# Kernel tuning notes

Measured on AMD Instinct MI355X. Metric: run time of the kernel, lower is better.

The kernel has to match this reference:

```python
import jax, jax.numpy as jnp
import numpy as np

B, N, D, H, E = 8, 2048, 128, 256, 524288
EPS = 1e-5

def setup_inputs() -> dict:
    key = jax.random.key(0)
    ks = jax.random.split(key, 16)
    def lin(k, fan_in, shape):
        b = 1.0 / np.sqrt(fan_in)
        return jax.random.uniform(k, shape, jnp.float32, -b, b)
    return {
        'x': jax.random.normal(ks[0], (B, N, 3), jnp.float32),
        'h': jax.random.normal(ks[1], (B, N, D), jnp.float32),
        'edge_indices': jax.random.randint(ks[2], (2, E), 0, B * N, jnp.int64),
        'batch_size': B,
        # filter_net: Linear(1,H) -> SiLU -> Linear(H,D)   (weights stored [in,out])
        'W1': lin(ks[3], 1, (1, H)), 'b1': lin(ks[4], 1, (H,)),
        'W2': lin(ks[5], H, (H, D)), 'b2': lin(ks[6], H, (D,)),
        # update_net: Linear(2D,H) -> LayerNorm(H) -> SiLU -> Linear(H,D)
        'W3': lin(ks[7], 2 * D, (2 * D, H)), 'b3': lin(ks[8], 2 * D, (H,)),
        'gamma': jnp.ones((H,), jnp.float32), 'beta': jnp.zeros((H,), jnp.float32),
        'W4': lin(ks[9], H, (H, D)), 'b4': lin(ks[10], H, (D,)),
    }

def reference(x, h, edge_indices, batch_size, W1, b1, W2, b2, W3, b3, gamma, beta, W4, b4):
    Bn, Nn, Dn = h.shape
    row, col = edge_indices[0], edge_indices[1]
    br, nr = row // Nn, row % Nn
    bc, nc = col // Nn, col % Nn
    x_row = x[br, nr]            # [E,3] gather
    x_col = x[bc, nc]            # [E,3]
    h_col = h[bc, nc]            # [E,D]
    diff = x_row - x_col
    dist = jnp.sqrt(jnp.sum(diff * diff, axis=-1, keepdims=True))  # [E,1]
    # distance-conditioned edge filter MLP
    edge_filters = jax.nn.silu(dist @ W1 + b1) @ W2 + b2           # [E,D]
    messages = h_col * edge_filters                                 # [E,D]
    # scatter-mean into B*N nodes (single-pass sum + count, clamp_min(1))
    n_tot = Bn * Nn
    sums = jax.ops.segment_sum(messages, row, num_segments=n_tot)
    counts = jax.ops.segment_sum(jnp.ones_like(row, dtype=messages.dtype), row, num_segments=n_tot)
    agg = (sums / jnp.maximum(counts, 1.0)[:, None]).reshape(Bn, Nn, Dn)
    # update MLP with LayerNorm
    u = jnp.concatenate([h, agg], axis=-1) @ W3 + b3               # [B,N,H]
    mu = jnp.mean(u, axis=-1, keepdims=True)
    var = jnp.mean((u - mu) ** 2, axis=-1, keepdims=True)
    un = (u - mu) * jax.lax.rsqrt(var + EPS) * gamma + beta
    return jax.nn.silu(un) @ W4 + b4                                # [B,N,D]
```

## Files before the change

kernel.cpp:

```cpp
#include <hip/hip_runtime.h>
#include <hip/hip_fp16.h>
#include <math.h>

#define BN_NODES 16384
#define DIM 128
#define HID 256
#define TK 4096
#define TRANGE 32.0f
#define TSTEP (TRANGE / (float)TK)
#define TINV  ((float)TK / TRANGE)
#define LN_EPS 1e-5f
#define EPB 4096
#define NBINS 1024
#define CAPB 768

typedef _Float16 f16x8 __attribute__((ext_vector_type(8)));
typedef __attribute__((ext_vector_type(4))) float f32x4;
typedef __attribute__((ext_vector_type(2))) float floatx2;
typedef __attribute__((ext_vector_type(8))) unsigned short ushort8v;

__device__ __forceinline__ unsigned short f2h(float f) {
    _Float16 h = (_Float16)f;
    return *(unsigned short*)&h;
}
__device__ __forceinline__ __half2 u2h2(unsigned int u) {
    union { unsigned int u; __half2 h; } c; c.u = u; return c.h;
}

__device__ __forceinline__ void edge_acc(unsigned int rec, int dd,
        const unsigned char* __restrict__ xq,
        const unsigned short* __restrict__ Tb, float& a0, float& a1) {
    int c = (int)((rec >> 12) & 0x3FFFu);
    int k = (int)(rec & 0xFFFu);
    unsigned short hq = *(const unsigned short*)&xq[c * DIM + dd];
    unsigned int tv = *(const unsigned int*)&Tb[k * DIM + dd];
    floatx2 hf = __builtin_amdgcn_cvt_pk_f32_fp8((int)hq, false);
    __half2 th = u2h2(tv);
    a0 = fmaf(hf[0], __low2float(th), a0);
    a1 = fmaf(hf[1], __high2float(th), a1);
}

__device__ __forceinline__ void node_tail(const unsigned int* lrec, int from, int to,
        int dd, const unsigned char* __restrict__ xq,
        const unsigned short* __restrict__ Tb, float& a0, float& a1) {
    int i = from;
    for (; i + 4 <= to; i += 4) {
        unsigned int e0 = lrec[i], e1 = lrec[i + 1], e2 = lrec[i + 2], e3 = lrec[i + 3];
        edge_acc(e0, dd, xq, Tb, a0, a1);
        edge_acc(e1, dd, xq, Tb, a0, a1);
        edge_acc(e2, dd, xq, Tb, a0, a1);
        edge_acc(e3, dd, xq, Tb, a0, a1);
    }
    for (; i < to; ++i) edge_acc(lrec[i], dd, xq, Tb, a0, a1);
}

__global__ __launch_bounds__(256) void prep_kernel(
        const float* __restrict__ W1, const float* __restrict__ b1,
        const float* __restrict__ W2, const float* __restrict__ b2,
        const float* __restrict__ W3, const float* __restrict__ W4,
        const float* __restrict__ h, const int* __restrict__ ei,
        const float* __restrict__ x,
        unsigned short* __restrict__ Tb, unsigned short* __restrict__ w3t,
        unsigned short* __restrict__ w4t, unsigned short* __restrict__ xh,
        unsigned char* __restrict__ xq, int* __restrict__ bin_cursor,
        unsigned int* __restrict__ staging, int nE) {
    __shared__ float smem[8 * 256 + 8 * 128];
    int bid = blockIdx.x, t = threadIdx.x;
    if (bid < 512) {
        float* a    = smem;
        float* part = smem + 8 * 256;
        int k0 = bid * 8;
        float w1 = W1[t], bb = b1[t];
#pragma unroll
        for (int k = 0; k < 8; ++k) {
            float dist = ((float)(k0 + k) + 0.5f) * TSTEP;
            float z = dist * w1 + bb;
            a[k * 256 + t] = z / (1.0f + expf(-z));
        }
        __syncthreads();
        int hg = t >> 7, d = t & 127;
        float acc[8] = {0.f,0.f,0.f,0.f,0.f,0.f,0.f,0.f};
        for (int hh = 0; hh < 128; ++hh) {
            int hidx = hg * 128 + hh;
            float w = W2[hidx * DIM + d];
#pragma unroll
            for (int k = 0; k < 8; ++k) acc[k] += a[k * 256 + hidx] * w;
        }
        if (hg == 1) {
#pragma unroll
            for (int k = 0; k < 8; ++k) part[k * 128 + d] = acc[k];
        }
        __syncthreads();
        if (hg == 0) {
            float bd = b2[d];
#pragma unroll
            for (int k = 0; k < 8; ++k)
                Tb[(k0 + k) * DIM + d] = f2h(acc[k] + part[k * 128 + d] + bd);
        }
    } else if (bid < 576) {
        float* s = smem;
        int tid = bid - 512, tr = tid >> 3, tc = tid & 7;
        int lr = t >> 5, lc = t & 31;
#pragma unroll
        for (int rep = 0; rep < 4; ++rep) {
            int k = tr * 32 + rep * 8 + lr, n = tc * 32 + lc;
            s[lc * 33 + rep * 8 + lr] = W3[k * 256 + n];
        }
        __syncthreads();
#pragma unroll
        for (int rep = 0; rep < 4; ++rep) {
            int n = tc * 32 + rep * 8 + lr, k = tr * 32 + lc;
            w3t[n * 256 + k] = f2h(s[(rep * 8 + lr) * 33 + lc]);
        }
    } else if (bid < 608) {
        float* s = smem;
        int tid = bid - 576, tr = tid >> 2, tc = tid & 3;
        int lr = t >> 5, lc = t & 31;
#pragma unroll
        for (int rep = 0; rep < 4; ++rep) {
            int k = tr * 32 + rep * 8 + lr, n = tc * 32 + lc;
            s[lc * 33 + rep * 8 + lr] = W4[k * 128 + n];
        }
        __syncthreads();
#pragma unroll
        for (int rep = 0; rep < 4; ++rep) {
            int n = tc * 32 + rep * 8 + lr, k = tr * 32 + lc;
            w4t[n * 256 + k] = f2h(s[(rep * 8 + lr) * 33 + lc]);
        }
    } else if (bid < 1632) {
        int i0 = (bid - 608) * 2048 + t * 8;
        float4 v0 = *(const float4*)&h[i0];
        float4 v1 = *(const float4*)&h[i0 + 4];
        ushort8v o;
        o[0] = f2h(v0.x); o[1] = f2h(v0.y); o[2] = f2h(v0.z); o[3] = f2h(v0.w);
        o[4] = f2h(v1.x); o[5] = f2h(v1.y); o[6] = f2h(v1.z); o[7] = f2h(v1.w);
        *(ushort8v*)&xh[i0] = o;
        unsigned int q0 = 0, q1 = 0;
        q0 = __builtin_amdgcn_cvt_pk_fp8_f32(v0.x, v0.y, q0, false);
        q0 = __builtin_amdgcn_cvt_pk_fp8_f32(v0.z, v0.w, q0, true);
        q1 = __builtin_amdgcn_cvt_pk_fp8_f32(v1.x, v1.y, q1, false);
        q1 = __builtin_amdgcn_cvt_pk_fp8_f32(v1.z, v1.w, q1, true);
        uint2 qq; qq.x = q0; qq.y = q1;
        *(uint2*)&xq[i0] = qq;
    } else {
        __shared__ int cnt[NBINS];
        __shared__ int pre[NBINS];
        __shared__ int gba[NBINS];
        __shared__ int sc[256];
        __shared__ unsigned int rec[EPB];
        int e0 = (bid - 1632) * EPB;
        int m = min(EPB, nE - e0);
        if (m < 0) m = 0;
#pragma unroll
        for (int j = 0; j < 4; ++j) cnt[j * 256 + t] = 0;
        __syncthreads();
        unsigned int code[16];
        int rk[16], bn[16];
#pragma unroll
        for (int j = 0; j < 16; ++j) {
            int idx = j * 256 + t;
            rk[j] = -1; bn[j] = 0; code[j] = 0;
            if (idx < m) {
                int e = e0 + idx;
                int r = ei[e], c = ei[nE + e];
                code[j] = ((unsigned int)r << 14) | (unsigned int)c;
                bn[j] = r >> 4;
                rk[j] = atomicAdd(&cnt[bn[j]], 1);
            }
        }
        __syncthreads();
        int c4[4], s4 = 0;
#pragma unroll
        for (int j = 0; j < 4; ++j) { c4[j] = cnt[t * 4 + j]; s4 += c4[j]; }
        sc[t] = s4;
        __syncthreads();
        for (int off = 1; off < 256; off <<= 1) {
            int v = (t >= off) ? sc[t - off] : 0;
            __syncthreads();
            sc[t] += v;
            __syncthreads();
        }
        int run = sc[t] - s4;
#pragma unroll
        for (int j = 0; j < 4; ++j) {
            int b = t * 4 + j;
            pre[b] = run; run += c4[j];
            gba[b] = atomicAdd(&bin_cursor[b], c4[j]);
        }
        __syncthreads();
#pragma unroll
        for (int j = 0; j < 16; ++j)
            if (rk[j] >= 0) rec[pre[bn[j]] + rk[j]] = code[j];
        __syncthreads();
        for (int i = t; i < m; i += 256) {
            unsigned int cd = rec[i];
            int b = (int)(cd >> 18);
            int r = (int)(cd >> 14);
            int c = (int)(cd & 0x3FFFu);
            float dx = x[r * 3 + 0] - x[c * 3 + 0];
            float dy = x[r * 3 + 1] - x[c * 3 + 1];
            float dz = x[r * 3 + 2] - x[c * 3 + 2];
            float u = sqrtf(dx * dx + dy * dy + dz * dz) * TINV;
            int k = min((int)u, TK - 1);
            unsigned int o = ((unsigned int)(r & 15) << 26)
                           | ((unsigned int)c << 12) | (unsigned int)k;
            int off = gba[b] + (i - pre[b]);
            if (off < CAPB) staging[b * CAPB + off] = o;
        }
    }
}

__global__ __launch_bounds__(512, 8) void mega_kernel(
        const unsigned int* __restrict__ staging, const int* __restrict__ bin_cursor,
        const unsigned short* __restrict__ Tb, const unsigned char* __restrict__ xq,
        const unsigned short* __restrict__ xh, const unsigned short* __restrict__ w3t,
        const float* __restrict__ b3, const float* __restrict__ gamma,
        const float* __restrict__ beta, const unsigned short* __restrict__ w4t,
        const float* __restrict__ b4, float* __restrict__ out) {
    __shared__ unsigned int lrec[CAPB];
    __shared__ int cnt16[16];
    __shared__ int pref[17];
    __shared__ int cur[16];
    __shared__ __align__(16) unsigned short aggh[16][136];
    __shared__ __align__(16) unsigned short a_lds[16][264];
    __shared__ float part_s[8][16], part_q[8][16];
    __shared__ float tot_mu[16], tot_rs[16];

    int t = threadIdx.x;
    int bin = blockIdx.x;
    int n0 = bin * 16;
    if (t < 16) cnt16[t] = 0;
    __syncthreads();
    int total = min(bin_cursor[bin], CAPB);
    long base = (long)bin * CAPB;

    unsigned int sr0 = 0, sr1 = 0;
    int have0 = (t < total), have1 = (t + 512 < total);
    if (have0) { sr0 = staging[base + t];       atomicAdd(&cnt16[sr0 >> 26], 1); }
    if (have1) { sr1 = staging[base + t + 512]; atomicAdd(&cnt16[sr1 >> 26], 1); }
    __syncthreads();
    if (t < 16) {
        int c = cnt16[t];
        int s = c;
#pragma unroll
        for (int off = 1; off < 16; off <<= 1) {
            int v = __shfl_up(s, off, 16);
            if (t >= off) s += v;
        }
        pref[t + 1] = s;
        cur[t] = s - c;
        if (t == 0) pref[0] = 0;
    }
    __syncthreads();

    if (have0) { int pos = atomicAdd(&cur[sr0 >> 26], 1); lrec[pos] = sr0; }
    if (have1) { int pos = atomicAdd(&cur[sr1 >> 26], 1); lrec[pos] = sr1; }
    __syncthreads();

    int wid = t >> 6, lane = t & 63, dd = lane * 2;

    {
        int j0 = wid * 2, j1 = j0 + 1;
        int off0 = pref[j0], len0 = pref[j0 + 1] - off0;
        int off1 = pref[j1], len1 = pref[j1 + 1] - off1;
        float a0x = 0.f, a0y = 0.f, a1x = 0.f, a1y = 0.f;
        int minl = min(len0, len1);
        int i = 0;
        for (; i + 8 <= minl; i += 8) {
#pragma unroll
            for (int u = 0; u < 8; ++u) {
                edge_acc(lrec[off0 + i + u], dd, xq, Tb, a0x, a0y);
                edge_acc(lrec[off1 + i + u], dd, xq, Tb, a1x, a1y);
            }
        }
        node_tail(lrec, off0 + i, off0 + len0, dd, xq, Tb, a0x, a0y);
        node_tail(lrec, off1 + i, off1 + len1, dd, xq, Tb, a1x, a1y);
        float inv0 = 1.0f / (float)max(len0, 1);
        float inv1 = 1.0f / (float)max(len1, 1);
        unsigned int p0 = (unsigned int)f2h(a0x * inv0) | ((unsigned int)f2h(a0y * inv0) << 16);
        unsigned int p1 = (unsigned int)f2h(a1x * inv1) | ((unsigned int)f2h(a1y * inv1) << 16);
        *(unsigned int*)&aggh[j0][dd] = p0;
        *(unsigned int*)&aggh[j1][dd] = p1;
    }
    __syncthreads();

    int wv = wid, q = lane >> 4, l15 = lane & 15;
    f32x4 acc[2];
    acc[0] = (f32x4){0.f, 0.f, 0.f, 0.f};
    acc[1] = (f32x4){0.f, 0.f, 0.f, 0.f};
    for (int kc = 0; kc < 8; ++kc) {
        f16x8 a;
        if (kc < 4) a = *(const f16x8*)&xh[(n0 + l15) * DIM + kc * 32 + q * 8];
        else        a = *(const f16x8*)&aggh[l15][(kc - 4) * 32 + q * 8];
#pragma unroll
        for (int nt = 0; nt < 2; ++nt) {
            f16x8 b = *(const f16x8*)&w3t[(wv * 32 + nt * 16 + l15) * 256 + kc * 32 + q * 8];
            acc[nt] = __builtin_amdgcn_mfma_f32_16x16x32_f16(a, b, acc[nt], 0, 0, 0);
        }
    }

    float b3v[2], gv[2], bvv[2];
#pragma unroll
    for (int nt = 0; nt < 2; ++nt) {
        int col = wv * 32 + nt * 16 + l15;
        b3v[nt] = b3[col]; gv[nt] = gamma[col]; bvv[nt] = beta[col];
    }
    {
        float s_[4], q_[4];
#pragma unroll
        for (int reg = 0; reg < 4; ++reg) {
            float su = 0.f, sq = 0.f;
#pragma unroll
            for (int nt = 0; nt < 2; ++nt) {
                float v = acc[nt][reg] + b3v[nt];
                acc[nt][reg] = v;
                su += v; sq += v * v;
            }
            s_[reg] = su; q_[reg] = sq;
        }
#pragma unroll
        for (int off = 1; off < 16; off <<= 1) {
#pragma unroll
            for (int reg = 0; reg < 4; ++reg) {
                s_[reg] += __shfl_xor(s_[reg], off, 64);
                q_[reg] += __shfl_xor(q_[reg], off, 64);
            }
        }
        if (l15 == 0) {
#pragma unroll
            for (int reg = 0; reg < 4; ++reg) {
                int r = q * 4 + reg;
                part_s[wv][r] = s_[reg];
                part_q[wv][r] = q_[reg];
            }
        }
    }
    __syncthreads();
    if (t < 16) {
        float st = 0.f, qt = 0.f;
#pragma unroll
        for (int w = 0; w < 8; ++w) { st += part_s[w][t]; qt += part_q[w][t]; }
        float mu = st * (1.0f / 256.0f);
        float var = qt * (1.0f / 256.0f) - mu * mu;
        tot_mu[t] = mu;
        tot_rs[t] = rsqrtf(var + LN_EPS);
    }
    __syncthreads();

#pragma unroll
    for (int reg = 0; reg < 4; ++reg) {
        int r = q * 4 + reg;
        float mu = tot_mu[r], rs = tot_rs[r];
#pragma unroll
        for (int nt = 0; nt < 2; ++nt) {
            float un = (acc[nt][reg] - mu) * rs * gv[nt] + bvv[nt];
            float act = un / (1.0f + expf(-un));
            a_lds[r][wv * 32 + nt * 16 + l15] = f2h(act);
        }
    }
    __syncthreads();

    f32x4 acc2 = (f32x4){0.f, 0.f, 0.f, 0.f};
    int col2 = wv * 16 + l15;
    for (int kc = 0; kc < 8; ++kc) {
        f16x8 a = *(const f16x8*)&a_lds[l15][kc * 32 + q * 8];
        f16x8 b = *(const f16x8*)&w4t[col2 * 256 + kc * 32 + q * 8];
        acc2 = __builtin_amdgcn_mfma_f32_16x16x32_f16(a, b, acc2, 0, 0, 0);
    }
    float b4v = b4[col2];
#pragma unroll
    for (int reg = 0; reg < 4; ++reg) {
        int node = n0 + q * 4 + reg;
        out[node * DIM + col2] = acc2[reg] + b4v;
    }
}

extern "C" void kernel_launch(void* const* d_in, const int* in_sizes, int n_in,
                              void* d_out, int out_size, void* d_ws, size_t ws_size,
                              hipStream_t stream) {
    const float* x     = (const float*)d_in[0];
    const float* h     = (const float*)d_in[1];
    const int*   ei    = (const int*)d_in[2];
    const float* W1    = (const float*)d_in[4];
    const float* b1    = (const float*)d_in[5];
    const float* W2    = (const float*)d_in[6];
    const float* b2    = (const float*)d_in[7];
    const float* W3    = (const float*)d_in[8];
    const float* b3    = (const float*)d_in[9];
    const float* gamma = (const float*)d_in[10];
    const float* beta  = (const float*)d_in[11];
    const float* W4    = (const float*)d_in[12];
    const float* b4    = (const float*)d_in[13];
    float* out = (float*)d_out;
    int nE = in_sizes[2] / 2;

    char* ws = (char*)d_ws;
    unsigned short* Tb   = (unsigned short*)ws; ws += (size_t)TK * DIM * 2;
    unsigned short* w3t  = (unsigned short*)ws; ws += (size_t)HID * HID * 2;
    unsigned short* w4t  = (unsigned short*)ws; ws += (size_t)DIM * HID * 2;
    unsigned short* xh   = (unsigned short*)ws; ws += (size_t)BN_NODES * DIM * 2;
    unsigned char*  xq   = (unsigned char*)ws;  ws += (size_t)BN_NODES * DIM;
    int* bin_cursor = (int*)ws;                 ws += (size_t)NBINS * 4;
    unsigned int* staging = (unsigned int*)ws;  ws += (size_t)NBINS * CAPB * 4;

    int binBlocks = (nE + EPB - 1) / EPB;
    hipMemsetAsync(bin_cursor, 0, (size_t)NBINS * 4, stream);
    prep_kernel<<<1632 + binBlocks, 256, 0, stream>>>(W1, b1, W2, b2, W3, W4, h, ei, x,
                                                      Tb, w3t, w4t, xh, xq,
                                                      bin_cursor, staging, nE);
    mega_kernel<<<NBINS, 512, 0, stream>>>(staging, bin_cursor, Tb, xq, xh,
                                           w3t, b3, gamma, beta, w4t, b4, out);
}
```

Baseline: 160.8 us.

## Vectorize edge gather to 8 features per lane with split-edge reduction

Restructures the per-node edge aggregation so each lane handles 8 feature channels with 64-bit fp8 and 128-bit fp16 table loads, instead of 2 channels with narrow loads. Four 16-lane groups each cover one node and half its edges, and the two halves are combined with a cross-lane shuffle. Staging reads and output writes use nontemporal hints. The wider loads reduce the number of memory instructions per edge. In exchange, fewer independent gathers are in flight per wave, and only half the lanes write results.

```diff
diff --git a/kernel.cpp b/kernel.cpp
--- a/kernel.cpp
+++ b/kernel.cpp
@@ -27,31 +27,20 @@
     union { unsigned int u; __half2 h; } c; c.u = u; return c.h;
 }
 
-__device__ __forceinline__ void edge_acc(unsigned int rec, int dd,
-        const unsigned char* __restrict__ xq,
-        const unsigned short* __restrict__ Tb, float& a0, float& a1) {
-    int c = (int)((rec >> 12) & 0x3FFFu);
-    int k = (int)(rec & 0xFFFu);
-    unsigned short hq = *(const unsigned short*)&xq[c * DIM + dd];
-    unsigned int tv = *(const unsigned int*)&Tb[k * DIM + dd];
-    floatx2 hf = __builtin_amdgcn_cvt_pk_f32_fp8((int)hq, false);
-    __half2 th = u2h2(tv);
-    a0 = fmaf(hf[0], __low2float(th), a0);
-    a1 = fmaf(hf[1], __high2float(th), a1);
-}
-
-__device__ __forceinline__ void node_tail(const unsigned int* lrec, int from, int to,
-        int dd, const unsigned char* __restrict__ xq,
-        const unsigned short* __restrict__ Tb, float& a0, float& a1) {
-    int i = from;
-    for (; i + 4 <= to; i += 4) {
-        unsigned int e0 = lrec[i], e1 = lrec[i + 1], e2 = lrec[i + 2], e3 = lrec[i + 3];
-        edge_acc(e0, dd, xq, Tb, a0, a1);
-        edge_acc(e1, dd, xq, Tb, a0, a1);
-        edge_acc(e2, dd, xq, Tb, a0, a1);
-        edge_acc(e3, dd, xq, Tb, a0, a1);
-    }
-    for (; i < to; ++i) edge_acc(lrec[i], dd, xq, Tb, a0, a1);
+__device__ __forceinline__ void acc8(uint2 q, uint4 tv, float* a) {
+    floatx2 h01 = __builtin_amdgcn_cvt_pk_f32_fp8((int)q.x, false);
+    floatx2 h23 = __builtin_amdgcn_cvt_pk_f32_fp8((int)q.x, true);
+    floatx2 h45 = __builtin_amdgcn_cvt_pk_f32_fp8((int)q.y, false);
+    floatx2 h67 = __builtin_amdgcn_cvt_pk_f32_fp8((int)q.y, true);
+    __half2 t01 = u2h2(tv.x), t23 = u2h2(tv.y), t45 = u2h2(tv.z), t67 = u2h2(tv.w);
+    a[0] = fmaf(h01[0], __low2float(t01),  a[0]);
+    a[1] = fmaf(h01[1], __high2float(t01), a[1]);
+    a[2] = fmaf(h23[0], __low2float(t23),  a[2]);
+    a[3] = fmaf(h23[1], __high2float(t23), a[3]);
+    a[4] = fmaf(h45[0], __low2float(t45),  a[4]);
+    a[5] = fmaf(h45[1], __high2float(t45), a[5]);
+    a[6] = fmaf(h67[0], __low2float(t67),  a[6]);
+    a[7] = fmaf(h67[1], __high2float(t67), a[7]);
 }
 
 __global__ __launch_bounds__(256) void prep_kernel(
@@ -236,8 +225,10 @@
 
     unsigned int sr0 = 0, sr1 = 0;
     int have0 = (t < total), have1 = (t + 512 < total);
-    if (have0) { sr0 = staging[base + t];       atomicAdd(&cnt16[sr0 >> 26], 1); }
-    if (have1) { sr1 = staging[base + t + 512]; atomicAdd(&cnt16[sr1 >> 26], 1); }
+    if (have0) { sr0 = __builtin_nontemporal_load(&staging[base + t]);
+                 atomicAdd(&cnt16[sr0 >> 26], 1); }
+    if (have1) { sr1 = __builtin_nontemporal_load(&staging[base + t + 512]);
+                 atomicAdd(&cnt16[sr1 >> 26], 1); }
     __syncthreads();
     if (t < 16) {
         int c = cnt16[t];
@@ -257,30 +248,43 @@
     if (have1) { int pos = atomicAdd(&cur[sr1 >> 26], 1); lrec[pos] = sr1; }
     __syncthreads();
 
-    int wid = t >> 6, lane = t & 63, dd = lane * 2;
+    int wid = t >> 6, lane = t & 63;
 
     {
-        int j0 = wid * 2, j1 = j0 + 1;
-        int off0 = pref[j0], len0 = pref[j0 + 1] - off0;
-        int off1 = pref[j1], len1 = pref[j1 + 1] - off1;
-        float a0x = 0.f, a0y = 0.f, a1x = 0.f, a1y = 0.f;
-        int minl = min(len0, len1);
-        int i = 0;
-        for (; i + 8 <= minl; i += 8) {
-#pragma unroll
-            for (int u = 0; u < 8; ++u) {
-                edge_acc(lrec[off0 + i + u], dd, xq, Tb, a0x, a0y);
-                edge_acc(lrec[off1 + i + u], dd, xq, Tb, a1x, a1y);
-            }
-        }
-        node_tail(lrec, off0 + i, off0 + len0, dd, xq, Tb, a0x, a0y);
-        node_tail(lrec, off1 + i, off1 + len1, dd, xq, Tb, a1x, a1y);
-        float inv0 = 1.0f / (float)max(len0, 1);
-        float inv1 = 1.0f / (float)max(len1, 1);
-        unsigned int p0 = (unsigned int)f2h(a0x * inv0) | ((unsigned int)f2h(a0y * inv0) << 16);
-        unsigned int p1 = (unsigned int)f2h(a1x * inv1) | ((unsigned int)f2h(a1y * inv1) << 16);
-        *(unsigned int*)&aggh[j0][dd] = p0;
-        *(unsigned int*)&aggh[j1][dd] = p1;
+        int g = lane >> 4, l16 = lane & 15, dd = l16 * 8;
+        int node = wid * 2 + (g >> 1);
+        int sub = g & 1;
+        int off = pref[node], len = pref[node + 1] - off;
+        float a[8] = {0.f,0.f,0.f,0.f,0.f,0.f,0.f,0.f};
+        int i = sub;
+        for (; i + 2 < len; i += 4) {
+            unsigned int r0 = lrec[off + i];
+            unsigned int r1 = lrec[off + i + 2];
+            int c0 = (int)((r0 >> 12) & 0x3FFFu), k0 = (int)(r0 & 0xFFFu);
+            int c1 = (int)((r1 >> 12) & 0x3FFFu), k1 = (int)(r1 & 0xFFFu);
+            uint2 q0 = *(const uint2*)&xq[c0 * DIM + dd];
+            uint4 t0 = *(const uint4*)&Tb[k0 * DIM + dd];
+            uint2 q1 = *(const uint2*)&xq[c1 * DIM + dd];
+            uint4 t1 = *(const uint4*)&Tb[k1 * DIM + dd];
+            acc8(q0, t0, a);
+            acc8(q1, t1, a);
+        }
+        if (i < len) {
+            unsigned int r0 = lrec[off + i];
+            int c0 = (int)((r0 >> 12) & 0x3FFFu), k0 = (int)(r0 & 0xFFFu);
+            uint2 q0 = *(const uint2*)&xq[c0 * DIM + dd];
+            uint4 t0 = *(const uint4*)&Tb[k0 * DIM + dd];
+            acc8(q0, t0, a);
+        }
+#pragma unroll
+        for (int r = 0; r < 8; ++r) a[r] += __shfl_xor(a[r], 16, 64);
+        if (sub == 0) {
+            float inv = 1.0f / (float)max(len, 1);
+            ushort8v o;
+#pragma unroll
+            for (int r = 0; r < 8; ++r) o[r] = f2h(a[r] * inv);
+            *(ushort8v*)&aggh[node][dd] = o;
+        }
     }
     __syncthreads();
 
@@ -371,7 +375,7 @@
 #pragma unroll
     for (int reg = 0; reg < 4; ++reg) {
         int node = n0 + q * 4 + reg;
-        out[node * DIM + col2] = acc2[reg] + b4v;
+        __builtin_nontemporal_store(acc2[reg] + b4v, &out[node * DIM + col2]);
     }
 }
 
```

New measurement: 159.1 us. No clear change (-1.0%).
